# Kernel optimization log

Measured on AMD Instinct MI355X. Metric: run time of the kernel, lower is better.

Reference implementation:

```python
import jax, jax.numpy as jnp
import numpy as np

B, N, F_IN, F_OUT = 8, 2048, 128, 128
NEG_BIG = -9e15
LEAKY_SLOPE = 0.01


def setup_inputs() -> dict:
    key = jax.random.key(0)
    k1, k2, k3, k4, k5 = jax.random.split(key, 5)
    features = jax.random.normal(k1, (B, N, F_IN), dtype=jnp.float32)
    adj_matrix = jax.random.randint(k2, (B, N, N), 0, 2, dtype=jnp.int32)
    mask = jnp.ones((B, N), dtype=jnp.float32)
    # linear: W [in,out], b [out]; attention: a [2*out] (no bias)
    W = jax.random.normal(k3, (F_IN, F_OUT), dtype=jnp.float32) / np.sqrt(F_IN)
    b = jnp.zeros((F_OUT,), dtype=jnp.float32)
    a = jax.random.normal(k4, (2 * F_OUT,), dtype=jnp.float32) / np.sqrt(2 * F_OUT)
    return {"features": features, "adj_matrix": adj_matrix, "mask": mask,
            "W": W, "b": b, "a": a}


def reference(features, adj_matrix, mask, W, b, a):
    h = jnp.einsum("bni,io->bno", features, W) + b  # [B,N,F_OUT]
    # attention(concat([h_i, h_j])) == h_i @ a_src + h_j @ a_dst
    a_src, a_dst = a[:F_OUT], a[F_OUT:]
    e = (h @ a_src)[:, :, None] + (h @ a_dst)[:, None, :]  # [B,N,N]
    e = jnp.where(e >= 0, e, LEAKY_SLOPE * e)  # leaky_relu
    scores = jnp.where(adj_matrix > 0, e, jnp.float32(NEG_BIG))
    attention = jax.nn.softmax(scores, axis=-1)
    aggregated = jnp.einsum("bnm,bmo->bno", attention, h)  # [B,N,F_OUT]
    aggregated = aggregated * mask[:, :, None]
    return aggregated
```

## Files before the change

kernel.cpp:

```cpp
#include <hip/hip_runtime.h>

#define BB 8
#define NN 2048
#define FF 128
#define ROWS 32
#define MT 128
#define PPAD 8

typedef short bh8 __attribute__((ext_vector_type(8)));
typedef float fl4 __attribute__((ext_vector_type(4)));
typedef unsigned short u16;

__device__ __forceinline__ u16 f2bf(float x) {
    unsigned u = __float_as_uint(x);
    return (u16)((u + 0x7FFFu + ((u >> 16) & 1u)) >> 16);
}

__global__ __launch_bounds__(256) void k_h(
    const float* __restrict__ feat, const float* __restrict__ W,
    const float* __restrict__ bias, const float* __restrict__ a,
    u16* __restrict__ htg, float* __restrict__ esrc, float* __restrict__ edst)
{
    __shared__ float fsh[8][FF];
    __shared__ float red[2][2][8];
    const int t = threadIdx.x;
    const long row0 = (long)blockIdx.x * 8;

    ((float4*)&fsh[0][0])[t] = ((const float4*)(feat + row0 * FF))[t];
    __syncthreads();

    const int o = t & 127;
    const int half = t >> 7;
    float acc[4] = {0.f, 0.f, 0.f, 0.f};
    #pragma unroll 4
    for (int k = 0; k < FF; ++k) {
        const float w = W[k * FF + o];
        #pragma unroll
        for (int r = 0; r < 4; ++r)
            acc[r] = fmaf(fsh[half * 4 + r][k], w, acc[r]);
    }
    const float bo = bias[o];
    const float as = a[o];
    const float ad = a[FF + o];
    float ps[4], pd[4];
    #pragma unroll
    for (int r = 0; r < 4; ++r) {
        acc[r] += bo;
        ps[r] = acc[r] * as;
        pd[r] = acc[r] * ad;
    }
    {
        const int bI = (int)(row0 >> 11);
        const int nloc = (int)(row0 & 2047) + half * 4;
        ushort4 hv;
        hv.x = f2bf(acc[0]); hv.y = f2bf(acc[1]);
        hv.z = f2bf(acc[2]); hv.w = f2bf(acc[3]);
        *(ushort4*)&htg[((long)bI * FF + o) * NN + nloc] = hv;
    }
    #pragma unroll
    for (int r = 0; r < 4; ++r) {
        #pragma unroll
        for (int off = 32; off > 0; off >>= 1) {
            ps[r] += __shfl_down(ps[r], off, 64);
            pd[r] += __shfl_down(pd[r], off, 64);
        }
    }
    const int wv = (t >> 6) & 1;
    if ((t & 63) == 0) {
        #pragma unroll
        for (int r = 0; r < 4; ++r) {
            red[half][wv][r]     = ps[r];
            red[half][wv][4 + r] = pd[r];
        }
    }
    __syncthreads();
    if (t < 16) {
        const int hh = t >> 3, idx = t & 7;
        const float v = red[hh][0][idx] + red[hh][1][idx];
        const long row = row0 + hh * 4 + (idx & 3);
        if (idx < 4) esrc[row] = v;
        else         edst[row] = v;
    }
}

__global__ __launch_bounds__(256) void k_gmax(
    const float* __restrict__ edst, float* __restrict__ gmax)
{
    const int b = blockIdx.x;
    const int t = threadIdx.x;
    float m = -1e30f;
    for (int i = t; i < NN; i += 256) m = fmaxf(m, edst[b * NN + i]);
    #pragma unroll
    for (int off = 32; off > 0; off >>= 1) m = fmaxf(m, __shfl_down(m, off, 64));
    __shared__ float sm[4];
    if ((t & 63) == 0) sm[t >> 6] = m;
    __syncthreads();
    if (t == 0) gmax[b] = fmaxf(fmaxf(sm[0], sm[1]), fmaxf(sm[2], sm[3]));
}

__global__ __launch_bounds__(512, 4) void k_attn(
    const int* __restrict__ adj, const float* __restrict__ mask,
    const u16* __restrict__ htg, const float* __restrict__ esrc,
    const float* __restrict__ edst, const float* __restrict__ gmax,
    float* __restrict__ out)
{
    __shared__ u16 p_sh[2][ROWS][MT + PPAD];
    __shared__ float psum_sh[ROWS];

    const int t = threadIdx.x;
    const int b = blockIdx.x & 7;
    const int n0 = (blockIdx.x >> 3) * ROWS;

    const int lane31 = t & 31;
    const int pr0 = (t >> 5) * 2;
    const long adjbase = (long)b * NN * NN + (long)(n0 + pr0) * NN;

    const float es0 = esrc[b * NN + n0 + pr0];
    const float es1 = esrc[b * NN + n0 + pr0 + 1];
    const float gm = gmax[b];
    const float t0 = es0 + gm; const float M0 = (t0 >= 0.f) ? t0 : 0.01f * t0;
    const float t1 = es1 + gm; const float M1 = (t1 >= 0.f) ? t1 : 0.01f * t1;

    const int w = t >> 6, lane = t & 63;
    const int rt = w & 1;
    const int c0 = (w >> 1) * 32;
    const int lr = lane & 15, g = lane >> 4;
    const u16* hB = htg + (long)b * FF * NN;

    fl4 acc0 = (fl4){0.f, 0.f, 0.f, 0.f};
    fl4 acc1 = (fl4){0.f, 0.f, 0.f, 0.f};
    float psum0 = 0.f, psum1 = 0.f;

    int4 adjv0 = *(const int4*)(adj + adjbase + lane31 * 4);
    int4 adjv1 = *(const int4*)(adj + adjbase + NN + lane31 * 4);
    float4 edv = *(const float4*)(edst + b * NN + lane31 * 4);

    int cur = 0;
    for (int m0 = 0; m0 < NN; m0 += MT) {
        bh8 bfrag[4][2];
        #pragma unroll
        for (int kc = 0; kc < 4; ++kc)
            #pragma unroll
            for (int ct = 0; ct < 2; ++ct)
                bfrag[kc][ct] = *(const bh8*)(hB + (long)(c0 + ct * 16 + lr) * NN
                                              + m0 + kc * 32 + g * 8);

        {
            const float edf[4] = {edv.x, edv.y, edv.z, edv.w};
            const int a0[4] = {adjv0.x, adjv0.y, adjv0.z, adjv0.w};
            const int a1[4] = {adjv1.x, adjv1.y, adjv1.z, adjv1.w};
            u16 pb0[4], pb1[4];
            #pragma unroll
            for (int j = 0; j < 4; ++j) {
                float x0 = es0 + edf[j]; x0 = (x0 >= 0.f) ? x0 : 0.01f * x0;
                float x1 = es1 + edf[j]; x1 = (x1 >= 0.f) ? x1 : 0.01f * x1;
                const float p0 = (a0[j] > 0) ? __expf(x0 - M0) : 0.f;
                const float p1 = (a1[j] > 0) ? __expf(x1 - M1) : 0.f;
                const u16 u0 = f2bf(p0), u1 = f2bf(p1);
                pb0[j] = u0; pb1[j] = u1;
                psum0 += __uint_as_float((unsigned)u0 << 16);
                psum1 += __uint_as_float((unsigned)u1 << 16);
            }
            *(ushort4*)&p_sh[cur][pr0][lane31 * 4]     = make_ushort4(pb0[0], pb0[1], pb0[2], pb0[3]);
            *(ushort4*)&p_sh[cur][pr0 + 1][lane31 * 4] = make_ushort4(pb1[0], pb1[1], pb1[2], pb1[3]);
        }

        {
            const int mn = (m0 + MT < NN) ? (m0 + MT) : m0;
            adjv0 = *(const int4*)(adj + adjbase + mn + lane31 * 4);
            adjv1 = *(const int4*)(adj + adjbase + NN + mn + lane31 * 4);
            edv   = *(const float4*)(edst + b * NN + mn + lane31 * 4);
        }

        asm volatile("s_waitcnt lgkmcnt(0)" ::: "memory");
        __builtin_amdgcn_s_barrier();
        asm volatile("" ::: "memory");

        #pragma unroll
        for (int kc = 0; kc < 4; ++kc) {
            const bh8 afrag = *(const bh8*)&p_sh[cur][16 * rt + lr][kc * 32 + g * 8];
            acc0 = __builtin_amdgcn_mfma_f32_16x16x32_bf16(afrag, bfrag[kc][0], acc0, 0, 0, 0);
            acc1 = __builtin_amdgcn_mfma_f32_16x16x32_bf16(afrag, bfrag[kc][1], acc1, 0, 0, 0);
        }
        cur ^= 1;
    }

    #pragma unroll
    for (int off = 16; off > 0; off >>= 1) {
        psum0 += __shfl_down(psum0, off, 32);
        psum1 += __shfl_down(psum1, off, 32);
    }
    if (lane31 == 0) { psum_sh[pr0] = psum0; psum_sh[pr0 + 1] = psum1; }
    __syncthreads();

    const long obase = ((long)b * NN + n0) * FF;
    #pragma unroll
    for (int reg = 0; reg < 4; ++reg) {
        const int rowin = 16 * rt + g * 4 + reg;
        const float s = mask[b * NN + n0 + rowin] / psum_sh[rowin];
        out[obase + (long)rowin * FF + c0 + lr]      = acc0[reg] * s;
        out[obase + (long)rowin * FF + c0 + 16 + lr] = acc1[reg] * s;
    }
}

extern "C" void kernel_launch(void* const* d_in, const int* in_sizes, int n_in,
                              void* d_out, int out_size, void* d_ws, size_t ws_size,
                              hipStream_t stream)
{
    const float* feat = (const float*)d_in[0];
    const int*   adj  = (const int*)d_in[1];
    const float* mask = (const float*)d_in[2];
    const float* W    = (const float*)d_in[3];
    const float* bias = (const float*)d_in[4];
    const float* a    = (const float*)d_in[5];
    float* out = (float*)d_out;

    u16*   htg  = (u16*)d_ws;
    float* esrc = (float*)(htg + (size_t)BB * FF * NN);
    float* edst = esrc + BB * NN;
    float* gmax = edst + BB * NN;

    k_h   <<<BB * NN / 8, 256, 0, stream>>>(feat, W, bias, a, htg, esrc, edst);
    k_gmax<<<BB,          256, 0, stream>>>(edst, gmax);
    k_attn<<<BB * (NN / ROWS), 512, 0, stream>>>(adj, mask, htg, esrc, edst, gmax, out);
}
```

Measured before the change: 92.56 us.

## Fuse global max into projection kernel, halve attention row block, deepen adj prefetch

Drops the separate gmax kernel: k_h now computes the per-batch edst max with an order-preserving atomicMax on unsigned-encoded floats, after a memset of the accumulator. The attention kernel moves from 32-row blocks of 512 threads to 16-row blocks of 256 threads, doubling the block count and doubling how often the h tiles are re-read across blocks. Adjacency and edst loads are prefetched two tiles ahead instead of one to hide global latency on the dominant adj stream. This adds an extra memset launch and atomics in exchange for one fewer kernel, and trades lower per-block reuse for more parallelism.

After: 112.9 us. 22.0% more time.

```diff
diff --git a/kernel.cpp b/kernel.cpp
--- a/kernel.cpp
+++ b/kernel.cpp
@@ -3,7 +3,7 @@
 #define BB 8
 #define NN 2048
 #define FF 128
-#define ROWS 32
+#define RB 16
 #define MT 128
 #define PPAD 8
 
@@ -19,7 +19,8 @@
 __global__ __launch_bounds__(256) void k_h(
     const float* __restrict__ feat, const float* __restrict__ W,
     const float* __restrict__ bias, const float* __restrict__ a,
-    u16* __restrict__ htg, float* __restrict__ esrc, float* __restrict__ edst)
+    u16* __restrict__ htg, float* __restrict__ esrc, float* __restrict__ edst,
+    unsigned* __restrict__ gmaxu)
 {
     __shared__ float fsh[8][FF];
     __shared__ float red[2][2][8];
@@ -80,36 +81,30 @@
         const long row = row0 + hh * 4 + (idx & 3);
         if (idx < 4) esrc[row] = v;
         else         edst[row] = v;
-    }
-}
-
-__global__ __launch_bounds__(256) void k_gmax(
-    const float* __restrict__ edst, float* __restrict__ gmax)
-{
-    const int b = blockIdx.x;
-    const int t = threadIdx.x;
-    float m = -1e30f;
-    for (int i = t; i < NN; i += 256) m = fmaxf(m, edst[b * NN + i]);
-    #pragma unroll
-    for (int off = 32; off > 0; off >>= 1) m = fmaxf(m, __shfl_down(m, off, 64));
-    __shared__ float sm[4];
-    if ((t & 63) == 0) sm[t >> 6] = m;
-    __syncthreads();
-    if (t == 0) gmax[b] = fmaxf(fmaxf(sm[0], sm[1]), fmaxf(sm[2], sm[3]));
-}
-
-__global__ __launch_bounds__(512, 4) void k_attn(
+        float mv = (idx >= 4) ? v : -3.4e38f;
+        #pragma unroll
+        for (int off = 8; off > 0; off >>= 1)
+            mv = fmaxf(mv, __shfl_xor(mv, off, 16));
+        if (t == 0) {
+            unsigned bu = __float_as_uint(mv);
+            bu = (bu & 0x80000000u) ? ~bu : (bu | 0x80000000u);
+            atomicMax(gmaxu + (int)(row0 >> 11), bu);
+        }
+    }
+}
+
+__global__ __launch_bounds__(256, 4) void k_attn(
     const int* __restrict__ adj, const float* __restrict__ mask,
     const u16* __restrict__ htg, const float* __restrict__ esrc,
-    const float* __restrict__ edst, const float* __restrict__ gmax,
+    const float* __restrict__ edst, const unsigned* __restrict__ gmaxu,
     float* __restrict__ out)
 {
-    __shared__ u16 p_sh[2][ROWS][MT + PPAD];
-    __shared__ float psum_sh[ROWS];
+    __shared__ u16 p_sh[2][RB][MT + PPAD];
+    __shared__ float psum_sh[RB];
 
     const int t = threadIdx.x;
     const int b = blockIdx.x & 7;
-    const int n0 = (blockIdx.x >> 3) * ROWS;
+    const int n0 = (blockIdx.x >> 3) * RB;
 
     const int lane31 = t & 31;
     const int pr0 = (t >> 5) * 2;
@@ -117,13 +112,13 @@
 
     const float es0 = esrc[b * NN + n0 + pr0];
     const float es1 = esrc[b * NN + n0 + pr0 + 1];
-    const float gm = gmax[b];
+    const unsigned gu = gmaxu[b];
+    const float gm = __uint_as_float((gu & 0x80000000u) ? (gu & 0x7FFFFFFFu) : ~gu);
     const float t0 = es0 + gm; const float M0 = (t0 >= 0.f) ? t0 : 0.01f * t0;
     const float t1 = es1 + gm; const float M1 = (t1 >= 0.f) ? t1 : 0.01f * t1;
 
     const int w = t >> 6, lane = t & 63;
-    const int rt = w & 1;
-    const int c0 = (w >> 1) * 32;
+    const int c0 = w * 32;
     const int lr = lane & 15, g = lane >> 4;
     const u16* hB = htg + (long)b * FF * NN;
 
@@ -131,9 +126,12 @@
     fl4 acc1 = (fl4){0.f, 0.f, 0.f, 0.f};
     float psum0 = 0.f, psum1 = 0.f;
 
-    int4 adjv0 = *(const int4*)(adj + adjbase + lane31 * 4);
-    int4 adjv1 = *(const int4*)(adj + adjbase + NN + lane31 * 4);
-    float4 edv = *(const float4*)(edst + b * NN + lane31 * 4);
+    int4 adjA0 = *(const int4*)(adj + adjbase + lane31 * 4);
+    int4 adjA1 = *(const int4*)(adj + adjbase + NN + lane31 * 4);
+    float4 edvA = *(const float4*)(edst + b * NN + lane31 * 4);
+    int4 adjB0 = *(const int4*)(adj + adjbase + MT + lane31 * 4);
+    int4 adjB1 = *(const int4*)(adj + adjbase + NN + MT + lane31 * 4);
+    float4 edvB = *(const float4*)(edst + b * NN + MT + lane31 * 4);
 
     int cur = 0;
     for (int m0 = 0; m0 < NN; m0 += MT) {
@@ -146,9 +144,9 @@
                                               + m0 + kc * 32 + g * 8);
 
         {
-            const float edf[4] = {edv.x, edv.y, edv.z, edv.w};
-            const int a0[4] = {adjv0.x, adjv0.y, adjv0.z, adjv0.w};
-            const int a1[4] = {adjv1.x, adjv1.y, adjv1.z, adjv1.w};
+            const float edf[4] = {edvA.x, edvA.y, edvA.z, edvA.w};
+            const int a0[4] = {adjA0.x, adjA0.y, adjA0.z, adjA0.w};
+            const int a1[4] = {adjA1.x, adjA1.y, adjA1.z, adjA1.w};
             u16 pb0[4], pb1[4];
             #pragma unroll
             for (int j = 0; j < 4; ++j) {
@@ -166,10 +164,11 @@
         }
 
         {
-            const int mn = (m0 + MT < NN) ? (m0 + MT) : m0;
-            adjv0 = *(const int4*)(adj + adjbase + mn + lane31 * 4);
-            adjv1 = *(const int4*)(adj + adjbase + NN + mn + lane31 * 4);
-            edv   = *(const float4*)(edst + b * NN + mn + lane31 * 4);
+            const int mn = (m0 + 2 * MT < NN) ? (m0 + 2 * MT) : 0;
+            adjA0 = adjB0; adjA1 = adjB1; edvA = edvB;
+            adjB0 = *(const int4*)(adj + adjbase + mn + lane31 * 4);
+            adjB1 = *(const int4*)(adj + adjbase + NN + mn + lane31 * 4);
+            edvB  = *(const float4*)(edst + b * NN + mn + lane31 * 4);
         }
 
         asm volatile("s_waitcnt lgkmcnt(0)" ::: "memory");
@@ -178,7 +177,7 @@
 
         #pragma unroll
         for (int kc = 0; kc < 4; ++kc) {
-            const bh8 afrag = *(const bh8*)&p_sh[cur][16 * rt + lr][kc * 32 + g * 8];
+            const bh8 afrag = *(const bh8*)&p_sh[cur][lr][kc * 32 + g * 8];
             acc0 = __builtin_amdgcn_mfma_f32_16x16x32_bf16(afrag, bfrag[kc][0], acc0, 0, 0, 0);
             acc1 = __builtin_amdgcn_mfma_f32_16x16x32_bf16(afrag, bfrag[kc][1], acc1, 0, 0, 0);
         }
@@ -196,7 +195,7 @@
     const long obase = ((long)b * NN + n0) * FF;
     #pragma unroll
     for (int reg = 0; reg < 4; ++reg) {
-        const int rowin = 16 * rt + g * 4 + reg;
+        const int rowin = g * 4 + reg;
         const float s = mask[b * NN + n0 + rowin] / psum_sh[rowin];
         out[obase + (long)rowin * FF + c0 + lr]      = acc0[reg] * s;
         out[obase + (long)rowin * FF + c0 + 16 + lr] = acc1[reg] * s;
@@ -218,9 +217,9 @@
     u16*   htg  = (u16*)d_ws;
     float* esrc = (float*)(htg + (size_t)BB * FF * NN);
     float* edst = esrc + BB * NN;
-    float* gmax = edst + BB * NN;
-
-    k_h   <<<BB * NN / 8, 256, 0, stream>>>(feat, W, bias, a, htg, esrc, edst);
-    k_gmax<<<BB,          256, 0, stream>>>(edst, gmax);
-    k_attn<<<BB * (NN / ROWS), 512, 0, stream>>>(adj, mask, htg, esrc, edst, gmax, out);
-}
+    unsigned* gmaxu = (unsigned*)(edst + BB * NN);
+
+    hipMemsetAsync(gmaxu, 0, BB * sizeof(unsigned), stream);
+    k_h   <<<BB * NN / 8, 256, 0, stream>>>(feat, W, bias, a, htg, esrc, edst, gmaxu);
+    k_attn<<<BB * (NN / RB), 256, 0, stream>>>(adj, mask, htg, esrc, edst, gmaxu, out);
+}
```
